# Kernel optimization log

Measured on AMD Instinct MI355X. Metric: run time of the kernel, lower is better.

## Reference

```python
import jax, jax.numpy as jnp
import numpy as np

W_CENTER_P = 1.0
W_CENTER_C = 1.0
EPS = 1e-6


def _adj_det3(S):
    """Analytic adjugate and determinant of batched 3x3 matrices (inverse-free)."""
    m00, m01, m02 = S[..., 0, 0], S[..., 0, 1], S[..., 0, 2]
    m10, m11, m12 = S[..., 1, 0], S[..., 1, 1], S[..., 1, 2]
    m20, m21, m22 = S[..., 2, 0], S[..., 2, 1], S[..., 2, 2]
    c00 = m11 * m22 - m12 * m21
    c01 = m02 * m21 - m01 * m22
    c02 = m01 * m12 - m02 * m11
    c10 = m12 * m20 - m10 * m22
    c11 = m00 * m22 - m02 * m20
    c12 = m02 * m10 - m00 * m12
    c20 = m10 * m21 - m11 * m20
    c21 = m01 * m20 - m00 * m21
    c22 = m00 * m11 - m01 * m10
    adj = jnp.stack([
        jnp.stack([c00, c01, c02], axis=-1),
        jnp.stack([c10, c11, c12], axis=-1),
        jnp.stack([c20, c21, c22], axis=-1),
    ], axis=-2)
    det = m00 * c00 + m01 * c01 + m02 * c02
    return adj, det


def _inv3(S):
    adj, det = _adj_det3(S)
    return adj / det[..., None, None]


def setup_inputs() -> dict:
    key = jax.random.key(0)
    k1, k2, k3, k4, k5 = jax.random.split(key, 5)
    B, N, K = 4, 4096, 512
    mu_child = jax.random.normal(k1, (B, N, 3), dtype=jnp.float32)
    mu_parent = jax.random.normal(k2, (B, K, 3), dtype=jnp.float32)
    Lc = jax.random.normal(k3, (B, N, 3, 3), dtype=jnp.float32)
    Lp = jax.random.normal(k4, (B, K, 3, 3), dtype=jnp.float32)
    eye = jnp.eye(3, dtype=jnp.float32)
    # SPD covariances: L L^T scaled + jitter
    Sigma_child = 0.1 * jnp.einsum('bnij,bnkj->bnik', Lc, Lc) + 0.1 * eye
    Sigma_parent = 0.1 * jnp.einsum('bkij,bklj->bkil', Lp, Lp) + 0.1 * eye
    A = jax.random.uniform(k5, (B, N, K), dtype=jnp.float32)
    mask = jnp.ones((B, N), dtype=jnp.float32)
    return {
        'mu_child': mu_child, 'Sigma_child': Sigma_child,
        'mu_parent': mu_parent, 'Sigma_parent': Sigma_parent,
        'A': A, 'mask': mask,
    }


def reference(mu_child, Sigma_child, mu_parent, Sigma_parent, A, mask):
    eye = jnp.eye(3, dtype=mu_child.dtype)
    # delta: [B, N, K, 3]
    delta = mu_child[:, :, None, :] - mu_parent[:, None, :, :]
    # Parent-side Mahalanobis via analytic 3x3 inverse kept at [B,K,3,3]
    inv_p = _inv3(Sigma_parent + EPS * eye)  # [B,K,3,3]
    maha_p = jnp.einsum('bnki,bkij,bnkj->bnk', delta, inv_p, delta)
    # fused_gaussian_overlap_score = -0.5 * maha; dist = -2 * score = maha
    dist_p = maha_p
    # Child-side, inverse at [B,N,3,3]
    inv_c = _inv3(Sigma_child + EPS * eye)  # [B,N,3,3]
    maha_c = jnp.einsum('bnki,bnij,bnkj->bnk', delta, inv_c, delta)
    dist_c = maha_c
    loss_matrix = W_CENTER_P * dist_p + W_CENTER_C * dist_c  # [B,N,K]
    denom = jnp.maximum(mask.sum(), 1.0)
    final_loss = ((loss_matrix * A).sum(axis=-1) * mask).sum() / denom
    dist_p_m = (dist_p * A * mask[..., None]).sum() / denom
    dist_c_m = (dist_c * A * mask[..., None]).sum() / denom
    return (final_loss, dist_p_m, dist_c_m)
```

## Files before the change

kernel.cpp:

```cpp
#include <hip/hip_runtime.h>

#define BB 4
#define NN 4096
#define KK 512
#define BLOCK 256
#define ROWS 16
#define GRID ((BB * NN) / ROWS)

static constexpr float W_P  = 1.0f;
static constexpr float W_C  = 1.0f;
static constexpr float EPSV = 1e-6f;

__device__ __forceinline__ void inv3_sym(const float* __restrict__ S,
                                         float& i00, float& i01, float& i02,
                                         float& i11, float& i12, float& i22) {
    float a00 = S[0] + EPSV, a01 = S[1], a02 = S[2];
    float a11 = S[4] + EPSV, a12 = S[5];
    float a22 = S[8] + EPSV;
    float c00 = a11 * a22 - a12 * a12;
    float c01 = a02 * a12 - a01 * a22;
    float c02 = a01 * a12 - a02 * a11;
    float c11 = a00 * a22 - a02 * a02;
    float c12 = a01 * a02 - a00 * a12;
    float c22 = a00 * a11 - a01 * a01;
    float det = a00 * c00 + a01 * c01 + a02 * c02;
    float r = 1.0f / det;
    i00 = c00 * r; i01 = c01 * r; i02 = c02 * r;
    i11 = c11 * r; i12 = c12 * r; i22 = c22 * r;
}

__global__ __launch_bounds__(BLOCK) void main_kernel(
        const float* __restrict__ mu_c, const float* __restrict__ Sg_c,
        const float* __restrict__ mu_p, const float* __restrict__ Sg_p,
        const float* __restrict__ A,    const float* __restrict__ mask,
        float* __restrict__ part) {
    __shared__ float4 sP0[KK];
    __shared__ float4 sP1[KK];
    __shared__ float  sP2[KK];
    __shared__ float4 sC0[ROWS];
    __shared__ float4 sC1[ROWS];
    __shared__ float  sC2[ROWS];
    __shared__ float  sM[ROWS];
    __shared__ float  red[8];

    const int tid = threadIdx.x;
    const int rowStart = blockIdx.x * ROWS;
    const int b = rowStart / NN;

    for (int k = tid; k < KK; k += BLOCK) {
        const int gp = b * KK + k;
        float i00, i01, i02, i11, i12, i22;
        inv3_sym(Sg_p + (size_t)gp * 9, i00, i01, i02, i11, i12, i22);
        const float* mu = mu_p + (size_t)gp * 3;
        sP0[k] = make_float4(mu[0], mu[1], mu[2], i00);
        sP1[k] = make_float4(2.0f * i01, 2.0f * i02, i11, 2.0f * i12);
        sP2[k] = i22;
    }
    if (tid < ROWS) {
        const int r = rowStart + tid;
        float i00, i01, i02, i11, i12, i22;
        inv3_sym(Sg_c + (size_t)r * 9, i00, i01, i02, i11, i12, i22);
        const float* mu = mu_c + (size_t)r * 3;
        sC0[tid] = make_float4(mu[0], mu[1], mu[2], i00);
        sC1[tid] = make_float4(2.0f * i01, 2.0f * i02, i11, 2.0f * i12);
        sC2[tid] = i22;
        sM[tid] = mask[r];
    }
    __syncthreads();

    float sp = 0.0f, sc = 0.0f;

    for (int rg = 0; rg < ROWS; rg += 2) {
        const float4 c0A = sC0[rg],     c0B = sC1[rg];
        const float  c0C = sC2[rg],     m0  = sM[rg];
        const float4 c1A = sC0[rg + 1], c1B = sC1[rg + 1];
        const float  c1C = sC2[rg + 1], m1  = sM[rg + 1];
        const float* __restrict__ A0 = A + (size_t)(rowStart + rg) * KK;
        const float* __restrict__ A1 = A0 + KK;

        #pragma unroll
        for (int ko = 0; ko < KK; ko += BLOCK) {
            const int k = ko + tid;
            const float4 p0 = sP0[k];
            const float4 p1 = sP1[k];
            const float  p2 = sP2[k];
            const float a0 = A0[k] * m0;
            const float a1 = A1[k] * m1;
            {
                float d0 = c0A.x - p0.x, d1 = c0A.y - p0.y, d2 = c0A.z - p0.z;
                float e00 = d0 * d0, e11 = d1 * d1, e22 = d2 * d2;
                float e01 = d0 * d1, e02 = d0 * d2, e12 = d1 * d2;
                float qp = p0.w * e00 + p1.z * e11 + p2 * e22
                         + p1.x * e01 + p1.y * e02 + p1.w * e12;
                float qc = c0A.w * e00 + c0B.z * e11 + c0C * e22
                         + c0B.x * e01 + c0B.y * e02 + c0B.w * e12;
                sp += qp * a0;
                sc += qc * a0;
            }
            {
                float d0 = c1A.x - p0.x, d1 = c1A.y - p0.y, d2 = c1A.z - p0.z;
                float e00 = d0 * d0, e11 = d1 * d1, e22 = d2 * d2;
                float e01 = d0 * d1, e02 = d0 * d2, e12 = d1 * d2;
                float qp = p0.w * e00 + p1.z * e11 + p2 * e22
                         + p1.x * e01 + p1.y * e02 + p1.w * e12;
                float qc = c1A.w * e00 + c1B.z * e11 + c1C * e22
                         + c1B.x * e01 + c1B.y * e02 + c1B.w * e12;
                sp += qp * a1;
                sc += qc * a1;
            }
        }
    }

    #pragma unroll
    for (int off = 32; off > 0; off >>= 1) {
        sp += __shfl_down(sp, off);
        sc += __shfl_down(sc, off);
    }
    const int wave = tid >> 6;
    if ((tid & 63) == 0) { red[wave * 2] = sp; red[wave * 2 + 1] = sc; }
    __syncthreads();
    if (tid == 0) {
        part[blockIdx.x]            = red[0] + red[2] + red[4] + red[6];
        part[GRID + blockIdx.x]     = red[1] + red[3] + red[5] + red[7];
        float msum = 0.0f;
        #pragma unroll
        for (int i = 0; i < ROWS; ++i) msum += sM[i];
        part[2 * GRID + blockIdx.x] = msum;
    }
}

__global__ __launch_bounds__(256) void finalize_kernel(
        const float* __restrict__ part, float* __restrict__ out) {
    __shared__ float red[12];
    const int tid = threadIdx.x;
    float tp = 0.0f, tc = 0.0f, tm = 0.0f;
    for (int i = tid; i < GRID; i += 256) {
        tp += part[i];
        tc += part[GRID + i];
        tm += part[2 * GRID + i];
    }
    #pragma unroll
    for (int off = 32; off > 0; off >>= 1) {
        tp += __shfl_down(tp, off);
        tc += __shfl_down(tc, off);
        tm += __shfl_down(tm, off);
    }
    const int wave = tid >> 6;
    if ((tid & 63) == 0) {
        red[wave * 3] = tp; red[wave * 3 + 1] = tc; red[wave * 3 + 2] = tm;
    }
    __syncthreads();
    if (tid == 0) {
        float sp = red[0] + red[3] + red[6] + red[9];
        float sc = red[1] + red[4] + red[7] + red[10];
        float sm = red[2] + red[5] + red[8] + red[11];
        float denom = fmaxf(sm, 1.0f);
        out[0] = (W_P * sp + W_C * sc) / denom;
        out[1] = sp / denom;
        out[2] = sc / denom;
    }
}

extern "C" void kernel_launch(void* const* d_in, const int* in_sizes, int n_in,
                              void* d_out, int out_size, void* d_ws, size_t ws_size,
                              hipStream_t stream) {
    const float* mu_c = (const float*)d_in[0];
    const float* Sg_c = (const float*)d_in[1];
    const float* mu_p = (const float*)d_in[2];
    const float* Sg_p = (const float*)d_in[3];
    const float* A    = (const float*)d_in[4];
    const float* mask = (const float*)d_in[5];
    float* out  = (float*)d_out;
    float* part = (float*)d_ws;

    main_kernel<<<GRID, BLOCK, 0, stream>>>(mu_c, Sg_c, mu_p, Sg_p, A, mask, part);
    finalize_kernel<<<1, 256, 0, stream>>>(part, out);
}
```

Measured before the change: 96.16 us.

## Hold parent params in registers and load A as float4 per thread

Each thread now owns four consecutive parent columns and keeps their center and inverse-covariance terms in registers for all its rows. The shared parent table is permuted so those loads stay conflict-free. Rows are split between the two half-blocks, and each row's A values are read with one float4 load instead of scalar loads. The goal is fewer shared-memory reloads and wider global loads, at the cost of more registers, with launch bounds set to keep occupancy.

```diff
diff --git a/kernel.cpp b/kernel.cpp
--- a/kernel.cpp
+++ b/kernel.cpp
@@ -29,14 +29,14 @@
     i11 = c11 * r; i12 = c12 * r; i22 = c22 * r;
 }
 
-__global__ __launch_bounds__(BLOCK) void main_kernel(
+__global__ __launch_bounds__(BLOCK, 4) void main_kernel(
         const float* __restrict__ mu_c, const float* __restrict__ Sg_c,
         const float* __restrict__ mu_p, const float* __restrict__ Sg_p,
         const float* __restrict__ A,    const float* __restrict__ mask,
         float* __restrict__ part) {
     __shared__ float4 sP0[KK];
     __shared__ float4 sP1[KK];
-    __shared__ float  sP2[KK];
+    __shared__ float4 sP2[KK / 4];
     __shared__ float4 sC0[ROWS];
     __shared__ float4 sC1[ROWS];
     __shared__ float  sC2[ROWS];
@@ -52,9 +52,10 @@
         float i00, i01, i02, i11, i12, i22;
         inv3_sym(Sg_p + (size_t)gp * 9, i00, i01, i02, i11, i12, i22);
         const float* mu = mu_p + (size_t)gp * 3;
-        sP0[k] = make_float4(mu[0], mu[1], mu[2], i00);
-        sP1[k] = make_float4(2.0f * i01, 2.0f * i02, i11, 2.0f * i12);
-        sP2[k] = i22;
+        const int idx = ((k & 3) << 7) | (k >> 2);
+        sP0[idx] = make_float4(mu[0], mu[1], mu[2], i00);
+        sP1[idx] = make_float4(2.0f * i01, 2.0f * i02, i11, 2.0f * i12);
+        ((float*)sP2)[k] = i22;
     }
     if (tid < ROWS) {
         const int r = rowStart + tid;
@@ -68,46 +69,43 @@
     }
     __syncthreads();
 
+    const int q = tid & 127;
+    const int h = tid >> 7;
+
+    float4 p0[4], p1[4];
+    #pragma unroll
+    for (int j = 0; j < 4; ++j) {
+        p0[j] = sP0[(j << 7) | q];
+        p1[j] = sP1[(j << 7) | q];
+    }
+    const float4 p2v = sP2[q];
+    const float p2a[4] = {p2v.x, p2v.y, p2v.z, p2v.w};
+
     float sp = 0.0f, sc = 0.0f;
+    const float* __restrict__ Abase = A + (size_t)rowStart * KK + (q << 2);
 
-    for (int rg = 0; rg < ROWS; rg += 2) {
-        const float4 c0A = sC0[rg],     c0B = sC1[rg];
-        const float  c0C = sC2[rg],     m0  = sM[rg];
-        const float4 c1A = sC0[rg + 1], c1B = sC1[rg + 1];
-        const float  c1C = sC2[rg + 1], m1  = sM[rg + 1];
-        const float* __restrict__ A0 = A + (size_t)(rowStart + rg) * KK;
-        const float* __restrict__ A1 = A0 + KK;
-
+    #pragma unroll
+    for (int rr = 0; rr < 8; ++rr) {
+        const int r = (h << 3) + rr;
+        const float4 cA = sC0[r];
+        const float4 cB = sC1[r];
+        const float  cC = sC2[r];
+        const float  m  = sM[r];
+        const float4 av = *reinterpret_cast<const float4*>(Abase + (size_t)r * KK);
+        const float aa[4] = {av.x * m, av.y * m, av.z * m, av.w * m};
         #pragma unroll
-        for (int ko = 0; ko < KK; ko += BLOCK) {
-            const int k = ko + tid;
-            const float4 p0 = sP0[k];
-            const float4 p1 = sP1[k];
-            const float  p2 = sP2[k];
-            const float a0 = A0[k] * m0;
-            const float a1 = A1[k] * m1;
-            {
-                float d0 = c0A.x - p0.x, d1 = c0A.y - p0.y, d2 = c0A.z - p0.z;
-                float e00 = d0 * d0, e11 = d1 * d1, e22 = d2 * d2;
-                float e01 = d0 * d1, e02 = d0 * d2, e12 = d1 * d2;
-                float qp = p0.w * e00 + p1.z * e11 + p2 * e22
-                         + p1.x * e01 + p1.y * e02 + p1.w * e12;
-                float qc = c0A.w * e00 + c0B.z * e11 + c0C * e22
-                         + c0B.x * e01 + c0B.y * e02 + c0B.w * e12;
-                sp += qp * a0;
-                sc += qc * a0;
-            }
-            {
-                float d0 = c1A.x - p0.x, d1 = c1A.y - p0.y, d2 = c1A.z - p0.z;
-                float e00 = d0 * d0, e11 = d1 * d1, e22 = d2 * d2;
-                float e01 = d0 * d1, e02 = d0 * d2, e12 = d1 * d2;
-                float qp = p0.w * e00 + p1.z * e11 + p2 * e22
-                         + p1.x * e01 + p1.y * e02 + p1.w * e12;
-                float qc = c1A.w * e00 + c1B.z * e11 + c1C * e22
-                         + c1B.x * e01 + c1B.y * e02 + c1B.w * e12;
-                sp += qp * a1;
-                sc += qc * a1;
-            }
+        for (int j = 0; j < 4; ++j) {
+            const float d0 = cA.x - p0[j].x;
+            const float d1 = cA.y - p0[j].y;
+            const float d2 = cA.z - p0[j].z;
+            const float e00 = d0 * d0, e11 = d1 * d1, e22 = d2 * d2;
+            const float e01 = d0 * d1, e02 = d0 * d2, e12 = d1 * d2;
+            const float qp = p0[j].w * e00 + p1[j].z * e11 + p2a[j] * e22
+                           + p1[j].x * e01 + p1[j].y * e02 + p1[j].w * e12;
+            const float qc = cA.w * e00 + cB.z * e11 + cC * e22
+                           + cB.x * e01 + cB.y * e02 + cB.w * e12;
+            sp += qp * aa[j];
+            sc += qc * aa[j];
         }
     }
 
```

Measured after the change: 140.3 us. +45.9%, slower.
